# Kernel tuning notes

Measured on AMD Instinct MI355X. Metric: run time of the kernel, lower is better.

The kernel has to match this reference:

```python
import jax, jax.numpy as jnp
import numpy as np

ADAPT_RATE = 0.05


def setup_inputs() -> dict:
    key = jax.random.key(0)
    k1, k2, k3 = jax.random.split(key, 3)
    B, T, DIN, DOUT = 64, 256, 1024, 1024
    x = jax.random.normal(k1, (B, T, DIN), dtype=jnp.float32)
    W = jax.random.normal(k2, (DOUT, DIN), dtype=jnp.float32) / np.sqrt(DIN)
    b = jax.random.normal(k3, (DOUT,), dtype=jnp.float32) * 0.01
    threshold = jnp.ones((DOUT,), dtype=jnp.float32)
    return {"x": x, "W": W, "b": b, "threshold": threshold}


def reference(x, W, b, threshold):
    # Precompute the per-timestep linear once as a single big GEMM: [B,T,O]
    pre = jnp.einsum('bti,oi->bto', x, W) + b
    B, T, O = pre.shape

    def step(carry, pre_t):
        mem, thr = carry
        mem = mem + pre_t                       # membrane accumulate [B,O]
        s = (mem >= thr).astype(pre_t.dtype)    # hard threshold spike
        # adaptive threshold: in-place .data update in torch (no grad path)
        thr = thr + ADAPT_RATE * (s.mean(axis=0) - 0.5)
        mem = mem * (1.0 - s)                   # reset where spiked
        return (mem, thr), s

    mem0 = jnp.zeros((B, O), dtype=x.dtype)
    (_, _), spikes = jax.lax.scan(step, (mem0, threshold), jnp.swapaxes(pre, 0, 1))
    return jnp.swapaxes(spikes, 0, 1)  # [B,T,O]
```

## Files before the change

### kernel.cpp

```cpp
#include <hip/hip_runtime.h>

#define B_ 64
#define T_ 256
#define DIN_ 1024
#define DOUT_ 1024

typedef int v4i  __attribute__((ext_vector_type(4)));
typedef int v16i __attribute__((ext_vector_type(16)));

#define PRE_BYTES 134217728ULL
#define XS_BYTES  83886080ULL
#define WSL_BYTES 5242880ULL
#define SPM_BYTES 2097152ULL

__device__ __forceinline__ void async_copy16(const void* g, void* l) {
    __builtin_amdgcn_global_load_lds(
        (const __attribute__((address_space(1))) void*)g,
        (__attribute__((address_space(3))) void*)l, 16, 0, 0);
}

__global__ __launch_bounds__(256) void snn_split_x(
    const float* __restrict__ x, char* __restrict__ xs)
{
    const int W    = blockIdx.x * 4 + (threadIdx.x >> 6);
    const int lane = threadIdx.x & 63;
    const int mt = W & 1, kt = (W >> 1) & 31, t0 = W >> 6;
    const int m = lane & 31, kh = lane >> 5;
    const int b = mt * 32 + m;

    const float* src = x + ((size_t)b * T_ + t0) * DIN_ + kt * 32 + kh * 16;
    float f[16];
    *(float4*)(f)      = *(const float4*)(src);
    *(float4*)(f + 4)  = *(const float4*)(src + 4);
    *(float4*)(f + 8)  = *(const float4*)(src + 8);
    *(float4*)(f + 12) = *(const float4*)(src + 12);

    unsigned pk[5][4];
#pragma unroll
    for (int s = 0; s < 5; ++s)
        pk[s][0] = pk[s][1] = pk[s][2] = pk[s][3] = 0u;
#pragma unroll
    for (int j = 0; j < 16; ++j) {
        float v = f[j] * 0.125f;
#pragma unroll
        for (int s = 0; s < 5; ++s) {
            const float ml = (s == 0) ? 64.f : 128.f;
            const float sv = __builtin_rintf(v * ml);
            v = v * ml - sv;
            const int iv = (int)sv;
            pk[s][j >> 2] |= ((unsigned)iv & 0xffu) << ((j & 3) * 8);
        }
    }
#pragma unroll
    for (int s = 0; s < 5; ++s) {
        char* dst = xs + (size_t)(((s * 256 + t0) * 32 + kt) * 2 + mt) * 1024
                       + lane * 16;
        *(uint4*)dst = make_uint4(pk[s][0], pk[s][1], pk[s][2], pk[s][3]);
    }
}

__global__ __launch_bounds__(256) void snn_split_w(
    const float* __restrict__ Wt, char* __restrict__ wsl)
{
    const int W    = blockIdx.x * 4 + (threadIdx.x >> 6);
    const int lane = threadIdx.x & 63;
    const int kt = W & 31, ot = W >> 5;
    const int n = lane & 31, kh = lane >> 5;
    const int o = ot * 32 + n;

    const float* src = Wt + (size_t)o * DIN_ + kt * 32 + kh * 16;
    float f[16];
    *(float4*)(f)      = *(const float4*)(src);
    *(float4*)(f + 4)  = *(const float4*)(src + 4);
    *(float4*)(f + 8)  = *(const float4*)(src + 8);
    *(float4*)(f + 12) = *(const float4*)(src + 12);

    unsigned pk[5][4];
#pragma unroll
    for (int s = 0; s < 5; ++s)
        pk[s][0] = pk[s][1] = pk[s][2] = pk[s][3] = 0u;
#pragma unroll
    for (int j = 0; j < 16; ++j) {
        float v = f[j] * 4.0f;
#pragma unroll
        for (int s = 0; s < 5; ++s) {
            const float ml = (s == 0) ? 64.f : 128.f;
            const float sv = __builtin_rintf(v * ml);
            v = v * ml - sv;
            const int iv = (int)sv;
            pk[s][j >> 2] |= ((unsigned)iv & 0xffu) << ((j & 3) * 8);
        }
    }
#pragma unroll
    for (int s = 0; s < 5; ++s) {
        char* dst = wsl + (size_t)((s * 32 + ot) * 32 + kt) * 1024 + lane * 16;
        *(uint4*)dst = make_uint4(pk[s][0], pk[s][1], pk[s][2], pk[s][3]);
    }
}

__global__ __launch_bounds__(256, 2) void snn_gemm_i8(
    const char* __restrict__ xs, const char* __restrict__ wsl,
    const float* __restrict__ bias, double* __restrict__ pre)
{
    __shared__ __align__(16) char lds[2][30 * 1024];
    const int t0 = blockIdx.x >> 3;
    const int oB = blockIdx.x & 7;
    const int tid = threadIdx.x;
    const int lane = tid & 63;
    const int ws = __builtin_amdgcn_readfirstlane(tid >> 6);
    const int wm  = ws >> 1;
    const int wop = (ws & 1) * 2;

    v16i zero;
#pragma unroll
    for (int r = 0; r < 16; ++r) zero[r] = 0;
    v16i acc[2][5];
#pragma unroll
    for (int p = 0; p < 2; ++p)
#pragma unroll
        for (int g = 0; g < 5; ++g) acc[p][g] = zero;

    const int lo = lane * 16;

    const char* agbase = xs + ((size_t)t0 * 32 * 2 + ws) * 1024;
    const char* bgbase = wsl + (size_t)(oB * 4 + (ws - 2) * 2) * 32 * 1024;

    if (ws < 2) {
#pragma unroll
        for (int s = 0; s < 5; ++s)
            async_copy16(agbase + (size_t)s * 16777216 + lo,
                         &lds[0][(ws * 5 + s) * 1024]);
    } else {
#pragma unroll
        for (int o2 = 0; o2 < 2; ++o2)
#pragma unroll
            for (int s = 0; s < 5; ++s)
                async_copy16(bgbase + (size_t)o2 * 32768 + (size_t)s * 1048576 + lo,
                             &lds[0][(10 + ((ws - 2) * 2 + o2) * 5 + s) * 1024]);
    }

    for (int kt = 0; kt < 32; ++kt) {
        __syncthreads();
        if (kt + 1 < 32) {
            char* buf = lds[(kt + 1) & 1];
            if (ws < 2) {
                const char* g = agbase + (size_t)(kt + 1) * 2048;
#pragma unroll
                for (int s = 0; s < 5; ++s)
                    async_copy16(g + (size_t)s * 16777216 + lo,
                                 &buf[(ws * 5 + s) * 1024]);
            } else {
                const char* g = bgbase + (size_t)(kt + 1) * 1024;
#pragma unroll
                for (int o2 = 0; o2 < 2; ++o2)
#pragma unroll
                    for (int s = 0; s < 5; ++s)
                        async_copy16(g + (size_t)o2 * 32768 + (size_t)s * 1048576 + lo,
                                     &buf[(10 + ((ws - 2) * 2 + o2) * 5 + s) * 1024]);
            }
        }
        const char* cbuf = lds[kt & 1];
        v4i a[5];
#pragma unroll
        for (int s = 0; s < 5; ++s)
            a[s] = *(const v4i*)(cbuf + (wm * 5 + s) * 1024 + lo);
#pragma unroll
        for (int o2 = 0; o2 < 2; ++o2) {
            v4i b[5];
#pragma unroll
            for (int s = 0; s < 5; ++s)
                b[s] = *(const v4i*)(cbuf + (10 + (wop + o2) * 5 + s) * 1024 + lo);
#pragma unroll
            for (int i = 0; i < 5; ++i) {
#pragma unroll
                for (int j = 0; j < 5 - i; ++j)
                    acc[o2][i + j] = __builtin_amdgcn_mfma_i32_32x32x32_i8(
                        a[i], b[j], acc[o2][i + j], 0, 0, 0);
            }
        }
    }

    const int n = lane & 31, lh = lane >> 5;
#pragma unroll
    for (int o2 = 0; o2 < 2; ++o2) {
        const int o = oB * 128 + (wop + o2) * 32 + n;
        const double bv = (double)bias[o];
        double* dst = pre + ((size_t)t0 * DOUT_ + o) * 64 + wm * 32;
#pragma unroll
        for (int r = 0; r < 16; ++r) {
            const int row = (r & 3) + 8 * (r >> 2) + 4 * lh;
            double v = (double)acc[o2][4][r];
            v = v * 0.0078125 + (double)acc[o2][3][r];
            v = v * 0.0078125 + (double)acc[o2][2][r];
            v = v * 0.0078125 + (double)acc[o2][1][r];
            v = v * 0.0078125 + (double)acc[o2][0][r];
            dst[row] = v * 0x1p-11 + bv;
        }
    }
}

__global__ __launch_bounds__(256, 2) void snn_gemm_fb(
    const float* __restrict__ x, const float* __restrict__ W,
    const float* __restrict__ bias, double* __restrict__ pre)
{
    __shared__ float smem[2][8 * 72 + 8 * 256];
    const int t0 = blockIdx.x & 255;
    const int o0 = blockIdx.x >> 8;
    const int tid = threadIdx.x;
    const int to = tid & 31;
    const int tb = tid >> 5;

    double acc[8][8];
#pragma unroll
    for (int i = 0; i < 8; ++i)
#pragma unroll
        for (int j = 0; j < 8; ++j) acc[i][j] = 0.0;

    const int arow = tid >> 2;
    const int ak2  = (tid & 3) * 2;
    const float* xg = x + (size_t)(t0 + 256 * arow) * DIN_ + ak2;
    const float* wg = W + (size_t)(o0 * 256 + tid) * DIN_;

    float2 f2  = *(const float2*)(xg);
    float4 bq0 = *(const float4*)(wg);
    float4 bq1 = *(const float4*)(wg + 4);

    for (int kc = 0; kc < DIN_ / 8; ++kc) {
        float* base = smem[kc & 1];
        float (*AsF)[72]  = (float(*)[72])base;
        float (*BsF)[256] = (float(*)[256])(base + 8 * 72);
        AsF[ak2 + 0][arow] = f2.x;
        AsF[ak2 + 1][arow] = f2.y;
        BsF[0][tid] = bq0.x;  BsF[1][tid] = bq0.y;
        BsF[2][tid] = bq0.z;  BsF[3][tid] = bq0.w;
        BsF[4][tid] = bq1.x;  BsF[5][tid] = bq1.y;
        BsF[6][tid] = bq1.z;  BsF[7][tid] = bq1.w;
        __syncthreads();
        if (kc + 1 < DIN_ / 8) {
            f2  = *(const float2*)(xg + (kc + 1) * 8);
            bq0 = *(const float4*)(wg + (kc + 1) * 8);
            bq1 = *(const float4*)(wg + (kc + 1) * 8 + 4);
        }
#pragma unroll
        for (int k = 0; k < 8; ++k) {
            const float4 af0 = *(const float4*)&AsF[k][tb * 8];
            const float4 af1 = *(const float4*)&AsF[k][tb * 8 + 4];
            const float4 bf0 = *(const float4*)&BsF[k][to * 4];
            const float4 bf1 = *(const float4*)&BsF[k][128 + to * 4];
            double a[8], b[8];
            a[0] = (double)af0.x; a[1] = (double)af0.y;
            a[2] = (double)af0.z; a[3] = (double)af0.w;
            a[4] = (double)af1.x; a[5] = (double)af1.y;
            a[6] = (double)af1.z; a[7] = (double)af1.w;
            b[0] = (double)bf0.x; b[1] = (double)bf0.y;
            b[2] = (double)bf0.z; b[3] = (double)bf0.w;
            b[4] = (double)bf1.x; b[5] = (double)bf1.y;
            b[6] = (double)bf1.z; b[7] = (double)bf1.w;
#pragma unroll
            for (int i = 0; i < 8; ++i)
#pragma unroll
                for (int j = 0; j < 8; ++j)
                    acc[i][j] += a[i] * b[j];
        }
    }

    double biasd[8];
#pragma unroll
    for (int j = 0; j < 8; ++j)
        biasd[j] = (double)bias[o0 * 256 + (j >> 2) * 128 + to * 4 + (j & 3)];
    double (*trans)[67] = (double(*)[67])smem[0];
    for (int c = 0; c < 16; ++c) {
        __syncthreads();
        const int j4  = c >> 3;
        const int tlo = (c & 7) * 4;
        if (to >= tlo && to < tlo + 4) {
#pragma unroll
            for (int p4 = 0; p4 < 4; ++p4) {
                const int r = (to - tlo) * 4 + p4;
                const int j = j4 * 4 + p4;
#pragma unroll
                for (int i = 0; i < 8; ++i)
                    trans[r][tb * 8 + i] = acc[i][j] + biasd[j];
            }
        }
        __syncthreads();
#pragma unroll
        for (int q = 0; q < 4; ++q) {
            const int idx = tid + 256 * q;
            const int b  = idx & 63;
            const int oc = idx >> 6;
            pre[(size_t)(t0 * DOUT_ + o0 * 256 + c * 16 + oc) * 64 + b] = trans[oc][b];
        }
    }
}

__global__ __launch_bounds__(256) void snn_scan(
    const double* __restrict__ pre, const float* __restrict__ thr_in,
    unsigned long long* __restrict__ spM, float* __restrict__ outD)
{
    const int wid  = (blockIdx.x * blockDim.x + threadIdx.x) >> 6;
    const int lane = threadIdx.x & 63;
    if (wid >= DOUT_) return;
    const int o = wid;

    double mem = 0.0;
    double thr = (double)thr_in[o];
    const double* p = pre + (size_t)o * 64 + lane;

    for (int t = 0; t < T_; t += 16) {
        double pv[16];
#pragma unroll
        for (int j = 0; j < 16; ++j)
            pv[j] = p[(size_t)(t + j) * (DOUT_ * 64)];
#pragma unroll
        for (int j = 0; j < 16; ++j) {
            mem += pv[j];
            const bool s = (mem >= thr);
            const unsigned long long msk = __ballot(s);
            const int cnt = __popcll(msk);
            thr += 0.05 * ((double)cnt * (1.0 / 64.0) - 0.5);
            if (spM) {
                if (lane == 0) spM[(size_t)(t + j) * DOUT_ + o] = msk;
            } else {
                outD[(size_t)lane * (T_ * DOUT_) + (size_t)(t + j) * DOUT_ + o] =
                    s ? 1.0f : 0.0f;
            }
            mem = s ? 0.0 : mem;
        }
    }
}

__global__ __launch_bounds__(256) void snn_expand(
    const unsigned long long* __restrict__ spM, float* __restrict__ out)
{
    const int r = blockIdx.x * 256 + threadIdx.x;
    const unsigned long long m = spM[r];
#pragma unroll
    for (int b = 0; b < 64; ++b)
        out[(size_t)b * (T_ * DOUT_) + r] = (float)((m >> b) & 1ULL);
}

extern "C" void kernel_launch(void* const* d_in, const int* in_sizes, int n_in,
                              void* d_out, int out_size, void* d_ws, size_t ws_size,
                              hipStream_t stream) {
    const float* x    = (const float*)d_in[0];
    const float* W    = (const float*)d_in[1];
    const float* bias = (const float*)d_in[2];
    const float* thr  = (const float*)d_in[3];
    float* out = (float*)d_out;

    double* pre = (double*)d_ws;
    const size_t need = PRE_BYTES + XS_BYTES + WSL_BYTES + SPM_BYTES;

    if (ws_size >= need) {
        char* xs  = (char*)d_ws + PRE_BYTES;
        char* wsl = xs + XS_BYTES;
        unsigned long long* spM = (unsigned long long*)(wsl + WSL_BYTES);
        snn_split_x<<<4096, 256, 0, stream>>>(x, xs);
        snn_split_w<<<256, 256, 0, stream>>>(W, wsl);
        snn_gemm_i8<<<2048, 256, 0, stream>>>(xs, wsl, bias, pre);
        snn_scan<<<256, 256, 0, stream>>>(pre, thr, spM, nullptr);
        snn_expand<<<1024, 256, 0, stream>>>(spM, out);
    } else {
        const bool two_stage = (ws_size >= PRE_BYTES + SPM_BYTES);
        unsigned long long* spM =
            two_stage ? (unsigned long long*)((char*)d_ws + PRE_BYTES) : nullptr;
        snn_gemm_fb<<<1024, 256, 0, stream>>>(x, W, bias, pre);
        snn_scan<<<256, 256, 0, stream>>>(pre, thr, spM, two_stage ? nullptr : out);
        if (two_stage)
            snn_expand<<<1024, 256, 0, stream>>>(spM, out);
    }
}
```

Before: 403.3 us.

## Load GEMM operands directly to registers, double-buffer scan loads, vectorize spike expand

The int8 split GEMM stops staging operands through double-buffered LDS with async copies and barriers. Each wave now loads its A and B fragments straight from global memory into registers, and the MFMA block runs under raised wave priority. The scan kernel double-buffers its 16-step prefetch of pre-activations so loads overlap the serial recurrence. The expand kernel writes float4 per thread with fewer blocks, and a missing barrier is added in the fallback GEMM. Dropping LDS staging removes sync overhead but relies on L2/L1 hits for operands reused across waves.

```diff
diff --git a/kernel.cpp b/kernel.cpp
--- a/kernel.cpp
+++ b/kernel.cpp
@@ -12,12 +12,6 @@
 #define XS_BYTES  83886080ULL
 #define WSL_BYTES 5242880ULL
 #define SPM_BYTES 2097152ULL
-
-__device__ __forceinline__ void async_copy16(const void* g, void* l) {
-    __builtin_amdgcn_global_load_lds(
-        (const __attribute__((address_space(1))) void*)g,
-        (__attribute__((address_space(3))) void*)l, 16, 0, 0);
-}
 
 __global__ __launch_bounds__(256) void snn_split_x(
     const float* __restrict__ x, char* __restrict__ xs)
@@ -102,7 +96,6 @@
     const char* __restrict__ xs, const char* __restrict__ wsl,
     const float* __restrict__ bias, double* __restrict__ pre)
 {
-    __shared__ __align__(16) char lds[2][30 * 1024];
     const int t0 = blockIdx.x >> 3;
     const int oB = blockIdx.x & 7;
     const int tid = threadIdx.x;
@@ -110,6 +103,7 @@
     const int ws = __builtin_amdgcn_readfirstlane(tid >> 6);
     const int wm  = ws >> 1;
     const int wop = (ws & 1) * 2;
+    const int lo  = lane * 16;
 
     v16i zero;
 #pragma unroll
@@ -120,64 +114,34 @@
 #pragma unroll
         for (int g = 0; g < 5; ++g) acc[p][g] = zero;
 
-    const int lo = lane * 16;
-
-    const char* agbase = xs + ((size_t)t0 * 32 * 2 + ws) * 1024;
-    const char* bgbase = wsl + (size_t)(oB * 4 + (ws - 2) * 2) * 32 * 1024;
-
-    if (ws < 2) {
+    const char* ab  = xs  + (size_t)(t0 * 64 + wm) * 1024 + lo;
+    const char* bb0 = wsl + (size_t)((oB * 4 + wop + 0) * 32) * 1024 + lo;
+    const char* bb1 = wsl + (size_t)((oB * 4 + wop + 1) * 32) * 1024 + lo;
+
+    for (int kt = 0; kt < 32; ++kt) {
+        v4i a[5], b0[5], b1[5];
 #pragma unroll
         for (int s = 0; s < 5; ++s)
-            async_copy16(agbase + (size_t)s * 16777216 + lo,
-                         &lds[0][(ws * 5 + s) * 1024]);
-    } else {
-#pragma unroll
-        for (int o2 = 0; o2 < 2; ++o2)
-#pragma unroll
-            for (int s = 0; s < 5; ++s)
-                async_copy16(bgbase + (size_t)o2 * 32768 + (size_t)s * 1048576 + lo,
-                             &lds[0][(10 + ((ws - 2) * 2 + o2) * 5 + s) * 1024]);
-    }
-
-    for (int kt = 0; kt < 32; ++kt) {
-        __syncthreads();
-        if (kt + 1 < 32) {
-            char* buf = lds[(kt + 1) & 1];
-            if (ws < 2) {
-                const char* g = agbase + (size_t)(kt + 1) * 2048;
-#pragma unroll
-                for (int s = 0; s < 5; ++s)
-                    async_copy16(g + (size_t)s * 16777216 + lo,
-                                 &buf[(ws * 5 + s) * 1024]);
-            } else {
-                const char* g = bgbase + (size_t)(kt + 1) * 1024;
-#pragma unroll
-                for (int o2 = 0; o2 < 2; ++o2)
-#pragma unroll
-                    for (int s = 0; s < 5; ++s)
-                        async_copy16(g + (size_t)o2 * 32768 + (size_t)s * 1048576 + lo,
-                                     &buf[(10 + ((ws - 2) * 2 + o2) * 5 + s) * 1024]);
+            a[s]  = *(const v4i*)(ab  + (size_t)s * 16777216 + kt * 2048);
+#pragma unroll
+        for (int s = 0; s < 5; ++s)
+            b0[s] = *(const v4i*)(bb0 + (size_t)s * 1048576 + kt * 1024);
+#pragma unroll
+        for (int s = 0; s < 5; ++s)
+            b1[s] = *(const v4i*)(bb1 + (size_t)s * 1048576 + kt * 1024);
+
+        __builtin_amdgcn_s_setprio(1);
+#pragma unroll
+        for (int i = 0; i < 5; ++i) {
+#pragma unroll
+            for (int j = 0; j < 5 - i; ++j) {
+                acc[0][i + j] = __builtin_amdgcn_mfma_i32_32x32x32_i8(
+                    a[i], b0[j], acc[0][i + j], 0, 0, 0);
+                acc[1][i + j] = __builtin_amdgcn_mfma_i32_32x32x32_i8(
+                    a[i], b1[j], acc[1][i + j], 0, 0, 0);
             }
         }
-        const char* cbuf = lds[kt & 1];
-        v4i a[5];
-#pragma unroll
-        for (int s = 0; s < 5; ++s)
-            a[s] = *(const v4i*)(cbuf + (wm * 5 + s) * 1024 + lo);
-#pragma unroll
-        for (int o2 = 0; o2 < 2; ++o2) {
-            v4i b[5];
-#pragma unroll
-            for (int s = 0; s < 5; ++s)
-                b[s] = *(const v4i*)(cbuf + (10 + (wop + o2) * 5 + s) * 1024 + lo);
-#pragma unroll
-            for (int i = 0; i < 5; ++i) {
-#pragma unroll
-                for (int j = 0; j < 5 - i; ++j)
-                    acc[o2][i + j] = __builtin_amdgcn_mfma_i32_32x32x32_i8(
-                        a[i], b[j], acc[o2][i + j], 0, 0, 0);
-            }
-        }
+        __builtin_amdgcn_s_setprio(0);
     }
 
     const int n = lane & 31, lh = lane >> 5;
@@ -262,6 +226,7 @@
                 for (int j = 0; j < 8; ++j)
                     acc[i][j] += a[i] * b[j];
         }
+        __syncthreads();
     }
 
     double biasd[8];
@@ -294,6 +259,31 @@
     }
 }
 
+#define SCAN_LOAD(PV, TB)                                                      \
+    do {                                                                       \
+        _Pragma("unroll")                                                      \
+        for (int j = 0; j < 16; ++j)                                           \
+            PV[j] = p[(size_t)((TB) + j) * (DOUT_ * 64)];                      \
+    } while (0)
+
+#define SCAN_STEP(PV, TB)                                                      \
+    do {                                                                       \
+        _Pragma("unroll")                                                      \
+        for (int j = 0; j < 16; ++j) {                                         \
+            mem += PV[j];                                                      \
+            const bool s = (mem >= thr);                                       \
+            const unsigned long long msk = __ballot(s);                        \
+            thr += 0.05 * ((double)__popcll(msk) * (1.0 / 64.0) - 0.5);        \
+            if (spM) {                                                         \
+                if (lane == 0) spM[(size_t)((TB) + j) * DOUT_ + o] = msk;      \
+            } else {                                                           \
+                outD[(size_t)lane * (T_ * DOUT_) +                             \
+                     (size_t)((TB) + j) * DOUT_ + o] = s ? 1.0f : 0.0f;        \
+            }                                                                  \
+            mem = s ? 0.0 : mem;                                               \
+        }                                                                      \
+    } while (0)
+
 __global__ __launch_bounds__(256) void snn_scan(
     const double* __restrict__ pre, const float* __restrict__ thr_in,
     unsigned long long* __restrict__ spM, float* __restrict__ outD)
@@ -307,37 +297,34 @@
     double thr = (double)thr_in[o];
     const double* p = pre + (size_t)o * 64 + lane;
 
-    for (int t = 0; t < T_; t += 16) {
-        double pv[16];
-#pragma unroll
-        for (int j = 0; j < 16; ++j)
-            pv[j] = p[(size_t)(t + j) * (DOUT_ * 64)];
-#pragma unroll
-        for (int j = 0; j < 16; ++j) {
-            mem += pv[j];
-            const bool s = (mem >= thr);
-            const unsigned long long msk = __ballot(s);
-            const int cnt = __popcll(msk);
-            thr += 0.05 * ((double)cnt * (1.0 / 64.0) - 0.5);
-            if (spM) {
-                if (lane == 0) spM[(size_t)(t + j) * DOUT_ + o] = msk;
-            } else {
-                outD[(size_t)lane * (T_ * DOUT_) + (size_t)(t + j) * DOUT_ + o] =
-                    s ? 1.0f : 0.0f;
-            }
-            mem = s ? 0.0 : mem;
-        }
+    double pvA[16], pvB[16];
+    SCAN_LOAD(pvA, 0);
+    for (int t = 0; t < T_; t += 32) {
+        if (t + 16 < T_) SCAN_LOAD(pvB, t + 16);
+        SCAN_STEP(pvA, t);
+        if (t + 32 < T_) SCAN_LOAD(pvA, t + 32);
+        SCAN_STEP(pvB, t + 16);
     }
 }
 
 __global__ __launch_bounds__(256) void snn_expand(
     const unsigned long long* __restrict__ spM, float* __restrict__ out)
 {
-    const int r = blockIdx.x * 256 + threadIdx.x;
-    const unsigned long long m = spM[r];
-#pragma unroll
-    for (int b = 0; b < 64; ++b)
-        out[(size_t)b * (T_ * DOUT_) + r] = (float)((m >> b) & 1ULL);
+    const int idx = blockIdx.x * 256 + threadIdx.x;
+    const int og = idx & 255;
+    const int t  = idx >> 8;
+    const unsigned long long* mp = spM + (size_t)t * DOUT_ + og * 4;
+    const unsigned long long m0 = mp[0], m1 = mp[1], m2 = mp[2], m3 = mp[3];
+    float* op = out + (size_t)t * DOUT_ + og * 4;
+#pragma unroll
+    for (int b = 0; b < 64; ++b) {
+        float4 v;
+        v.x = (float)((m0 >> b) & 1ULL);
+        v.y = (float)((m1 >> b) & 1ULL);
+        v.z = (float)((m2 >> b) & 1ULL);
+        v.w = (float)((m3 >> b) & 1ULL);
+        *(float4*)(op + (size_t)b * (T_ * DOUT_)) = v;
+    }
 }
 
 extern "C" void kernel_launch(void* const* d_in, const int* in_sizes, int n_in,
@@ -360,7 +347,7 @@
         snn_split_w<<<256, 256, 0, stream>>>(W, wsl);
         snn_gemm_i8<<<2048, 256, 0, stream>>>(xs, wsl, bias, pre);
         snn_scan<<<256, 256, 0, stream>>>(pre, thr, spM, nullptr);
-        snn_expand<<<1024, 256, 0, stream>>>(spM, out);
+        snn_expand<<<256, 256, 0, stream>>>(spM, out);
     } else {
         const bool two_stage = (ws_size >= PRE_BYTES + SPM_BYTES);
         unsigned long long* spM =
@@ -368,6 +355,6 @@
         snn_gemm_fb<<<1024, 256, 0, stream>>>(x, W, bias, pre);
         snn_scan<<<256, 256, 0, stream>>>(pre, thr, spM, two_stage ? nullptr : out);
         if (two_stage)
-            snn_expand<<<1024, 256, 0, stream>>>(spM, out);
-    }
-}
+            snn_expand<<<256, 256, 0, stream>>>(spM, out);
+    }
+}
```

New measurement: 419.8 us. 4.1% more time.
